# Optimization experiments

Hardware: AMD Instinct MI355X
Metric: run time of the kernel (lower is better)

Reference implementation:

```python
import jax, jax.numpy as jnp
import numpy as np

C = 1024
H = 16
K = 2  # num_states
B, N = 4, 4096


def setup_inputs() -> dict:
    key = jax.random.key(0)
    ks_ = jax.random.split(key, 12)
    s = 1.0 / np.sqrt(C)
    inp = {
        "x": jax.random.normal(ks_[0], (B, N, C), dtype=jnp.float32),
        "Wq": jax.random.normal(ks_[1], (C, C), dtype=jnp.float32) * s,
        "bq": jnp.zeros((C,), dtype=jnp.float32),
        "Wk": jax.random.normal(ks_[2], (K, C, C), dtype=jnp.float32) * s,
        "bk": jnp.zeros((K, C), dtype=jnp.float32),
        "Wv": jax.random.normal(ks_[3], (K, C, C), dtype=jnp.float32) * s,
        "bv": jnp.zeros((K, C), dtype=jnp.float32),
        "Wo": jax.random.normal(ks_[4], (C, C), dtype=jnp.float32) * s,
        "bo": jnp.zeros((C,), dtype=jnp.float32),
        "ln_g": jnp.ones((C,), dtype=jnp.float32),
        "ln_b": jnp.zeros((C,), dtype=jnp.float32),
    }
    return inp


def _heads(t):
    # [..., n, (h d)] -> [..., h, n, d]
    shp = t.shape
    d = shp[-1] // H
    t = t.reshape(shp[:-1] + (H, d))
    return jnp.swapaxes(t, -2, -3)


def reference(x, Wq, bq, Wk, bk, Wv, bv, Wo, bo, ln_g, ln_b):
    dtype = x.dtype
    # residual single-layer projections (ResidualMLP with num_layers=-1)
    q = x + jnp.einsum('bnc,cd->bnd', x, Wq) + bq
    ks = x[None] + jnp.einsum('bnc,kcd->kbnd', x, Wk) + bk[:, None, None, :]
    vs = x[None] + jnp.einsum('bnc,kcd->kbnd', x, Wv) + bv[:, None, None, :]
    q = _heads(q)        # [b,h,n,d]
    ks = _heads(ks)      # [k,b,h,n,d]
    vs = _heads(vs)      # [k,b,h,n,d]
    scale = 1.0 / jnp.sqrt(jnp.asarray(N, dtype=jnp.float32))
    ks = ks.astype(jnp.float32) * scale
    vs = vs.astype(jnp.float32) * scale
    # per-state KV outer-products: [k,b,h,d,e]
    states = jnp.einsum('kbhnd,kbhne->kbhde', ks, vs)
    state = jnp.prod(states, axis=0)  # [b,h,d,e]
    out = jnp.einsum('bhnd,bhde->bhne', q.astype(jnp.float32), state)
    out = out.astype(dtype)
    # [b,h,n,d] -> [b,n,(h d)]
    out = jnp.swapaxes(out, 1, 2).reshape(x.shape[0], x.shape[1], C)
    # LayerNorm
    mu = jnp.mean(out, axis=-1, keepdims=True)
    var = jnp.var(out, axis=-1, keepdims=True)
    out = (out - mu) / jnp.sqrt(var + 1e-5) * ln_g + ln_b
    out = jnp.einsum('bnc,cd->bnd', out, Wo) + bo
    return out
```

## Files before the change

### kernel.cpp

```cpp
#include <hip/hip_runtime.h>
#include <hip/hip_bf16.h>

typedef __attribute__((ext_vector_type(8))) short bf16x8;
typedef __attribute__((ext_vector_type(4))) float f32x4;
typedef __attribute__((ext_vector_type(4))) short s16x4;

__device__ __forceinline__ short f2bf(float f) {
  union { float f; unsigned u; } v; v.f = f;
  unsigned r = v.u + 0x7fffu + ((v.u >> 16) & 1u);
  return (short)(r >> 16);
}

__device__ __forceinline__ float bf2f(short s) {
  union { float f; unsigned u; } v; v.u = ((unsigned)(unsigned short)s) << 16;
  return v.f;
}

#define GLD_LDS(g, l) __builtin_amdgcn_global_load_lds( \
    (const __attribute__((address_space(1))) void*)(g), \
    (__attribute__((address_space(3))) void*)(l), 16, 0, 0)

__global__ __launch_bounds__(256)
void convt_k(const float* __restrict__ x, short* __restrict__ xb,
             short* __restrict__ xbT) {
  __shared__ short tile[64][72];
  const int b = blockIdx.z;
  const int n0 = blockIdx.y * 64;
  const int c0 = blockIdx.x * 64;
  const int t = threadIdx.x;
  const int nl = t >> 4;
  const int c4 = (t & 15) << 2;
  const float* xp = x + ((size_t)b * 4096 + n0) * 1024 + c0;
#pragma unroll
  for (int i = 0; i < 4; ++i) {
    const int n = nl + 16 * i;
    const float4 v = *(const float4*)(xp + (size_t)n * 1024 + c4);
    s16x4 o;
    o[0] = f2bf(v.x); o[1] = f2bf(v.y); o[2] = f2bf(v.z); o[3] = f2bf(v.w);
    *(s16x4*)(&xb[((size_t)b * 4096 + n0 + n) * 1024 + c0 + c4]) = o;
    *(s16x4*)(&tile[n][c4]) = o;
  }
  __syncthreads();
  const int cll = t >> 4;
  const int n4 = (t & 15) << 2;
#pragma unroll
  for (int i = 0; i < 4; ++i) {
    const int c = cll + 16 * i;
    s16x4 o;
    o[0] = tile[n4 + 0][c]; o[1] = tile[n4 + 1][c];
    o[2] = tile[n4 + 2][c]; o[3] = tile[n4 + 3][c];
    *(s16x4*)(&xbT[((size_t)b * 1024 + c0 + c) * 4096 + n0 + n4]) = o;
  }
}

__global__ void twc_k(const float* __restrict__ Wq, const float* __restrict__ Wk,
                      const float* __restrict__ Wv, const float* __restrict__ Wo,
                      const float* __restrict__ lng, short* __restrict__ dst) {
  __shared__ float tile[32][33];
  const int z = blockIdx.z;
  const float* src = (z == 0) ? Wq
                   : (z == 1) ? Wk
                   : (z == 2) ? (Wk + 1048576)
                   : (z == 3) ? Wv
                   : (z == 4) ? (Wv + 1048576)
                   : Wo;
  short* d = dst + (size_t)z * 1048576;
  const int tx = threadIdx.x, ty = threadIdx.y;
  const int c0 = blockIdx.y * 32, d0 = blockIdx.x * 32;
#pragma unroll
  for (int i = 0; i < 4; ++i)
    tile[ty + i * 8][tx] = src[(size_t)(c0 + ty + i * 8) * 1024 + d0 + tx];
  __syncthreads();
#pragma unroll
  for (int i = 0; i < 4; ++i) {
    const int cc = c0 + tx;
    const int dd = d0 + ty + i * 8;
    float v = tile[tx][ty + i * 8];
    if (z < 5) {
      if (cc == dd) v += 1.0f;
    } else {
      v *= lng[cc];
    }
    d[(size_t)dd * 1024 + cc] = f2bf(v);
  }
}

__global__ __launch_bounds__(256)
void colsumT_k(const short* __restrict__ xbT, float* __restrict__ s) {
  const int row = blockIdx.x;
  const int tid = threadIdx.x;
  const short* p = xbT + ((size_t)row << 12);
  float acc = 0.f;
#pragma unroll
  for (int it = 0; it < 2; ++it) {
    const bf16x8 v = *(const bf16x8*)(p + ((tid + it * 256) << 3));
#pragma unroll
    for (int j = 0; j < 8; ++j) acc += bf2f(v[j]);
  }
#pragma unroll
  for (int o = 32; o > 0; o >>= 1) acc += __shfl_down(acc, o);
  __shared__ float red[4];
  if ((tid & 63) == 0) red[tid >> 6] = acc;
  __syncthreads();
  if (tid == 0) s[row] = red[0] + red[1] + red[2] + red[3];
}

__global__ __launch_bounds__(256)
void gemv_k(const short* __restrict__ wt, const float* __restrict__ s,
            float* __restrict__ u, float* __restrict__ w) {
  const int z = blockIdx.z, b = blockIdx.y;
  const int lane = threadIdx.x & 63, wid = threadIdx.x >> 6;
  const short* W = wt + ((size_t)(z + 1) << 20);
  const float* sb = s + b * 1024;
  float* outp = (z < 2) ? (u + (z * 4 + b) * 1024) : (w + ((z - 2) * 4 + b) * 1024);
#pragma unroll 1
  for (int it = 0; it < 16; ++it) {
    const int d = blockIdx.x * 64 + wid * 16 + it;
    const short* row = W + (size_t)d * 1024 + lane * 16;
    float acc = 0.f;
#pragma unroll
    for (int j = 0; j < 16; ++j) acc += bf2f(row[j]) * sb[lane * 16 + j];
#pragma unroll
    for (int o = 32; o > 0; o >>= 1) acc += __shfl_down(acc, o);
    if (lane == 0) outp[d] = acc;
  }
}

__global__ __launch_bounds__(512, 2)
void gramq_k(const short* __restrict__ xb, const short* __restrict__ xbT,
             const short* __restrict__ wtq, const float* __restrict__ bq,
             short* __restrict__ q, float* __restrict__ Pg) {
  extern __shared__ short lds[];
  const int tid = threadIdx.x;
  const int lane = tid & 63;
  const int wv = tid >> 6;
  const int wm = wv >> 2;
  const int wn = wv & 3;
  const int mode = blockIdx.x & 1;
  const int id = blockIdx.x >> 1;
  const int swz = ((id & 7) << 5) + (id >> 3);

  int bm0, bn0, ld, koff;
  const short *Ap, *Bp;
  float* po = nullptr;
  if (mode == 0) {
    const int kz = swz & 3, tl = (swz >> 2) & 15, b = swz >> 6;
    bm0 = (tl >> 2) << 8; bn0 = (tl & 3) << 8;
    ld = 4096; koff = kz << 10;
    Ap = xbT + ((size_t)b << 22);
    Bp = Ap;
    po = Pg + ((size_t)((kz << 2) + b) << 20);
  } else {
    bm0 = (swz & 63) << 8; bn0 = (swz >> 6) << 8;
    ld = 1024; koff = 0;
    Ap = xb; Bp = wtq;
  }

  const int lrow = ((lane >> 3) << 1) | ((lane >> 2) & 1);
  const int kc = ((lane & 3) ^ ((lane >> 3) & 3)) << 3;
  const int cl = lane & 15;
  const int khi = lane >> 4;

  f32x4 acc[8][4];
#pragma unroll
  for (int i = 0; i < 8; ++i)
#pragma unroll
    for (int j = 0; j < 4; ++j) acc[i][j] = f32x4{0.f, 0.f, 0.f, 0.f};

  auto stage = [&](int buf, int t) {
    const int k0 = koff + (t << 5) + kc;
    short* ab = lds + (buf << 14);
    short* bb = ab + 8192;
#pragma unroll
    for (int c = 0; c < 2; ++c) {
      const int un = wv * 2 + c;
      GLD_LDS(Ap + (size_t)(bm0 + (un << 4) + lrow) * ld + k0, ab + (un << 9));
      GLD_LDS(Bp + (size_t)(bn0 + (un << 4) + lrow) * ld + k0, bb + (un << 9));
    }
  };

  auto compute = [&](int buf) {
    const short* ab = lds + (buf << 14);
    const short* bb = ab + 8192;
    bf16x8 af[8], bfr[4];
#pragma unroll
    for (int i = 0; i < 8; ++i) {
      const int R = (wm << 7) + (i << 4) + cl;
      af[i] = *(const bf16x8*)(ab + (R << 5) + ((khi ^ ((R >> 1) & 3)) << 3));
    }
#pragma unroll
    for (int j = 0; j < 4; ++j) {
      const int C = (wn << 6) + (j << 4) + cl;
      bfr[j] = *(const bf16x8*)(bb + (C << 5) + ((khi ^ ((C >> 1) & 3)) << 3));
    }
#pragma unroll
    for (int i = 0; i < 8; ++i)
#pragma unroll
      for (int j = 0; j < 4; ++j)
        acc[i][j] = __builtin_amdgcn_mfma_f32_16x16x32_bf16(af[i], bfr[j], acc[i][j], 0, 0, 0);
  };

  stage(0, 0);
  stage(1, 1);
  asm volatile("s_waitcnt vmcnt(4)" ::: "memory");
  __builtin_amdgcn_s_barrier();
#pragma unroll 1
  for (int t = 0; t < 30; ++t) {
    stage((t + 2) & 3, t + 2);
    compute(t & 3);
    asm volatile("s_waitcnt vmcnt(4)" ::: "memory");
    __builtin_amdgcn_s_barrier();
  }
  compute(2);
  asm volatile("s_waitcnt vmcnt(0)" ::: "memory");
  __builtin_amdgcn_s_barrier();
  compute(3);

  if (mode == 0) {
#pragma unroll
    for (int i = 0; i < 8; ++i)
#pragma unroll
      for (int j = 0; j < 4; ++j) {
        const int col = bn0 + (wn << 6) + (j << 4) + cl;
        const int rowb = bm0 + (wm << 7) + (i << 4) + (khi << 2);
#pragma unroll
        for (int r = 0; r < 4; ++r)
          po[(size_t)(rowb + r) * 1024 + col] = acc[i][j][r];
      }
  } else {
#pragma unroll
    for (int i = 0; i < 8; ++i)
#pragma unroll
      for (int j = 0; j < 4; ++j) {
        const int col = bn0 + (wn << 6) + (j << 4) + cl;
        const int rowb = bm0 + (wm << 7) + (i << 4) + (khi << 2);
        const float bi = bq[col];
#pragma unroll
        for (int r = 0; r < 4; ++r)
          q[(size_t)(rowb + r) * 1024 + col] = f2bf(acc[i][j][r] + bi);
      }
  }
}

__global__ __launch_bounds__(512, 2)
void gemmo_k(const short* __restrict__ A, const short* __restrict__ WT,
             const float* __restrict__ mu, const float* __restrict__ rstd,
             const float* __restrict__ uu, const float* __restrict__ tt,
             float* __restrict__ fout) {
  extern __shared__ short lds[];
  const int tid = threadIdx.x;
  const int lane = tid & 63;
  const int wv = tid >> 6;
  const int wm = wv >> 2;
  const int wn = wv & 3;
  const int swz = ((blockIdx.x & 7) << 5) + (blockIdx.x >> 3);
  const int bm0 = (swz & 63) << 8;
  const int bn0 = (swz >> 6) << 8;

  const int lrow = ((lane >> 3) << 1) | ((lane >> 2) & 1);
  const int kc = ((lane & 3) ^ ((lane >> 3) & 3)) << 3;
  const int cl = lane & 15;
  const int khi = lane >> 4;

  f32x4 acc[8][4];
#pragma unroll
  for (int i = 0; i < 8; ++i)
#pragma unroll
    for (int j = 0; j < 4; ++j) acc[i][j] = f32x4{0.f, 0.f, 0.f, 0.f};

  auto stage = [&](int buf, int t) {
    const int k0 = (t << 5) + kc;
    short* ab = lds + (buf << 14);
    short* bb = ab + 8192;
#pragma unroll
    for (int c = 0; c < 2; ++c) {
      const int un = wv * 2 + c;
      GLD_LDS(A + (size_t)(bm0 + (un << 4) + lrow) * 1024 + k0, ab + (un << 9));
      GLD_LDS(WT + (size_t)(bn0 + (un << 4) + lrow) * 1024 + k0, bb + (un << 9));
    }
  };

  auto compute = [&](int buf) {
    const short* ab = lds + (buf << 14);
    const short* bb = ab + 8192;
    bf16x8 af[8], bfr[4];
#pragma unroll
    for (int i = 0; i < 8; ++i) {
      const int R = (wm << 7) + (i << 4) + cl;
      af[i] = *(const bf16x8*)(ab + (R << 5) + ((khi ^ ((R >> 1) & 3)) << 3));
    }
#pragma unroll
    for (int j = 0; j < 4; ++j) {
      const int C = (wn << 6) + (j << 4) + cl;
      bfr[j] = *(const bf16x8*)(bb + (C << 5) + ((khi ^ ((C >> 1) & 3)) << 3));
    }
#pragma unroll
    for (int i = 0; i < 8; ++i)
#pragma unroll
      for (int j = 0; j < 4; ++j)
        acc[i][j] = __builtin_amdgcn_mfma_f32_16x16x32_bf16(af[i], bfr[j], acc[i][j], 0, 0, 0);
  };

  stage(0, 0);
  stage(1, 1);
  asm volatile("s_waitcnt vmcnt(4)" ::: "memory");
  __builtin_amdgcn_s_barrier();
#pragma unroll 1
  for (int t = 0; t < 30; ++t) {
    stage((t + 2) & 3, t + 2);
    compute(t & 3);
    asm volatile("s_waitcnt vmcnt(4)" ::: "memory");
    __builtin_amdgcn_s_barrier();
  }
  compute(2);
  asm volatile("s_waitcnt vmcnt(0)" ::: "memory");
  __builtin_amdgcn_s_barrier();
  compute(3);

#pragma unroll
  for (int i = 0; i < 8; ++i) {
    const int rowb = bm0 + (wm << 7) + (i << 4) + (khi << 2);
    const float4 m4 = *(const float4*)(mu + rowb);
    const float4 s4 = *(const float4*)(rstd + rowb);
#pragma unroll
    for (int j = 0; j < 4; ++j) {
      const int col = bn0 + (wn << 6) + (j << 4) + cl;
      const float uc = uu[col];
      const float tc = tt[col];
      fout[(size_t)(rowb + 0) * 1024 + col] = s4.x * (acc[i][j][0] - m4.x * uc) + tc;
      fout[(size_t)(rowb + 1) * 1024 + col] = s4.y * (acc[i][j][1] - m4.y * uc) + tc;
      fout[(size_t)(rowb + 2) * 1024 + col] = s4.z * (acc[i][j][2] - m4.z * uc) + tc;
      fout[(size_t)(rowb + 3) * 1024 + col] = s4.w * (acc[i][j][3] - m4.w * uc) + tc;
    }
  }
}

__global__ __launch_bounds__(256)
void greduce_k(const float* __restrict__ Pg, short* __restrict__ G) {
  const int b = blockIdx.x >> 10;
  const int local = ((blockIdx.x & 1023) << 10) + (threadIdx.x << 2);
  float4 a = {0.f, 0.f, 0.f, 0.f};
#pragma unroll
  for (int kz = 0; kz < 4; ++kz) {
    const float4 v = *(const float4*)(Pg + (((size_t)((kz << 2) + b)) << 20) + local);
    a.x += v.x; a.y += v.y; a.z += v.z; a.w += v.w;
  }
  const float sc = 1.0f / 4096.0f;
  s16x4 o;
  o[0] = f2bf(a.x * sc); o[1] = f2bf(a.y * sc);
  o[2] = f2bf(a.z * sc); o[3] = f2bf(a.w * sc);
  *(s16x4*)(G + ((size_t)b << 20) + local) = o;
}

__global__ __launch_bounds__(256)
void gemm128_k(const short* __restrict__ A, const short* __restrict__ Bt,
               short* __restrict__ out) {
  __shared__ short Ab[2][4096];
  __shared__ short Bb[2][4096];
  const int bid = blockIdx.x;
  const int swz = ((bid & 7) << 4) + (bid >> 3);
  const int bm0 = (swz >> 3) << 7;
  const int bn0 = (swz & 7) << 7;
  const short* Bp = Bt + ((size_t)blockIdx.y << 20);
  short* op = out + ((size_t)blockIdx.y << 21);
  const int tid = threadIdx.x, lane = tid & 63, wid = tid >> 6;
  const int wm = (wid >> 1) << 6, wn = (wid & 1) << 6;
  const int lrow = ((lane >> 3) << 1) | ((lane >> 2) & 1);
  const int kc = ((lane & 3) ^ ((lane >> 3) & 3)) << 3;
  const int cl = lane & 15, khi = lane >> 4;

  f32x4 acc[4][4];
#pragma unroll
  for (int i = 0; i < 4; ++i)
#pragma unroll
    for (int j = 0; j < 4; ++j) acc[i][j] = f32x4{0.f, 0.f, 0.f, 0.f};

  auto stage = [&](int buf, int t) {
    const int k0 = (t << 5) + kc;
#pragma unroll
    for (int c = 0; c < 2; ++c) {
      const int un = wid * 2 + c;
      GLD_LDS(A + (size_t)(bm0 + (un << 4) + lrow) * 1024 + k0, &Ab[buf][un << 9]);
      GLD_LDS(Bp + (size_t)(bn0 + (un << 4) + lrow) * 1024 + k0, &Bb[buf][un << 9]);
    }
  };

  stage(0, 0);
  __syncthreads();
#pragma unroll 1
  for (int t = 0; t < 32; ++t) {
    const int cur = t & 1;
    if (t < 31) stage(cur ^ 1, t + 1);
    const short* ab = Ab[cur];
    const short* bb = Bb[cur];
    bf16x8 af[4], bfr[4];
#pragma unroll
    for (int i = 0; i < 4; ++i) {
      const int R = wm + (i << 4) + cl;
      af[i] = *(const bf16x8*)(ab + (R << 5) + ((khi ^ ((R >> 1) & 3)) << 3));
    }
#pragma unroll
    for (int j = 0; j < 4; ++j) {
      const int C = wn + (j << 4) + cl;
      bfr[j] = *(const bf16x8*)(bb + (C << 5) + ((khi ^ ((C >> 1) & 3)) << 3));
    }
#pragma unroll
    for (int i = 0; i < 4; ++i)
#pragma unroll
      for (int j = 0; j < 4; ++j)
        acc[i][j] = __builtin_amdgcn_mfma_f32_16x16x32_bf16(af[i], bfr[j], acc[i][j], 0, 0, 0);
    __syncthreads();
  }

#pragma unroll
  for (int i = 0; i < 4; ++i)
#pragma unroll
    for (int j = 0; j < 4; ++j) {
      const int col = bn0 + wn + (j << 4) + cl;
      const int rowb = bm0 + wm + (i << 4) + (khi << 2);
#pragma unroll
      for (int r = 0; r < 4; ++r)
        op[(size_t)(rowb + r) * 1024 + col] = f2bf(acc[i][j][r]);
    }
}

__global__ __launch_bounds__(256)
void states2_k(const short* __restrict__ wt, const short* __restrict__ Tt,
               float* __restrict__ M) {
  __shared__ short Al[64 * 40];
  __shared__ short Bl[64 * 40];
  const int h = blockIdx.x, b = blockIdx.y, k = blockIdx.z;
  const short* Ap = wt + ((size_t)(1 + k) << 20) + ((size_t)(h * 64) << 10);
  const short* Bp = Tt + ((size_t)b << 21) + ((size_t)(k * 1024 + h * 64) << 10);
  const int tid = threadIdx.x, lane = tid & 63, wid = tid >> 6;
  const int srow = tid >> 2, sch = (tid & 3) << 3;

  f32x4 acc[4];
#pragma unroll
  for (int j = 0; j < 4; ++j) acc[j] = f32x4{0.f, 0.f, 0.f, 0.f};

#pragma unroll 1
  for (int ns = 0; ns < 1024; ns += 32) {
    bf16x8 va = *(const bf16x8*)(Ap + ((size_t)srow << 10) + ns + sch);
    bf16x8 vb = *(const bf16x8*)(Bp + ((size_t)srow << 10) + ns + sch);
    __syncthreads();
    *(bf16x8*)(Al + srow * 40 + sch) = va;
    *(bf16x8*)(Bl + srow * 40 + sch) = vb;
    __syncthreads();
    bf16x8 a = *(const bf16x8*)(Al + (wid * 16 + (lane & 15)) * 40 + ((lane >> 4) << 3));
#pragma unroll
    for (int j = 0; j < 4; ++j) {
      bf16x8 bb = *(const bf16x8*)(Bl + (j * 16 + (lane & 15)) * 40 + ((lane >> 4) << 3));
      acc[j] = __builtin_amdgcn_mfma_f32_16x16x32_bf16(a, bb, acc[j], 0, 0, 0);
    }
  }
  const size_t mb = ((size_t)((k * 4 + b) * 16 + h)) << 12;
  const int r0 = wid * 16 + ((lane >> 4) << 2);
  const int cl = lane & 15;
#pragma unroll
  for (int j = 0; j < 4; ++j)
#pragma unroll
    for (int r = 0; r < 4; ++r)
      M[mb + (size_t)(r0 + r) * 64 + j * 16 + cl] = acc[j][r];
}

__global__ __launch_bounds__(256)
void combine_k(const float* __restrict__ M, const float* __restrict__ u,
               const float* __restrict__ w, const float* __restrict__ bk,
               const float* __restrict__ bv, short* __restrict__ stt) {
  const int bh = blockIdx.x;
  const int b = bh >> 4, h = bh & 15;
  const float invN = 1.0f / 4096.0f;
  for (int t = threadIdx.x; t < 4096; t += 256) {
    const int d = t >> 6, e = t & 63;
    float m[2];
#pragma unroll
    for (int k = 0; k < 2; ++k) {
      const float bkd = bk[k * 1024 + h * 64 + d];
      const float bve = bv[k * 1024 + h * 64 + e];
      const float ud = u[(k * 4 + b) * 1024 + h * 64 + d];
      const float we = w[(k * 4 + b) * 1024 + h * 64 + e];
      m[k] = M[(((size_t)((k * 4 + b) * 16 + h)) << 12) + t]
           + (ud * bve + bkd * we + 4096.f * bkd * bve) * invN;
    }
    stt[(bh << 12) + (e << 6) + d] = f2bf(m[0] * m[1]);
  }
}

__global__ __launch_bounds__(256)
void ut_k(const float* __restrict__ Wo, const float* __restrict__ lng,
          const float* __restrict__ lnb, const float* __restrict__ bo,
          float* __restrict__ u, float* __restrict__ t) {
  const int dl = threadIdx.x & 63;
  const int dd = blockIdx.x * 64 + dl;
  const int part = threadIdx.x >> 6;
  float su = 0.f, st = 0.f;
  for (int c = part * 256; c < part * 256 + 256; ++c) {
    const float w = Wo[(size_t)c * 1024 + dd];
    su += lng[c] * w;
    st += lnb[c] * w;
  }
  __shared__ float rs[4][64], rt[4][64];
  rs[part][dl] = su; rt[part][dl] = st;
  __syncthreads();
  if (part == 0) {
    su = rs[0][dl] + rs[1][dl] + rs[2][dl] + rs[3][dl];
    st = rt[0][dl] + rt[1][dl] + rt[2][dl] + rt[3][dl];
    u[dd] = su;
    t[dd] = st + bo[dd];
  }
}

__global__ __launch_bounds__(256)
void attn_k(const short* __restrict__ q, const short* __restrict__ stt,
            short* __restrict__ oat) {
  __shared__ short Al[128 * 72];
  __shared__ short Bl[64 * 72];
  const int tid = threadIdx.x;
  const int lane = tid & 63;
  const int wid = tid >> 6;
  const int mc = blockIdx.x;
  const int bh = blockIdx.y;
  const int b = bh >> 4, h = bh & 15;
  const size_t qbase = ((size_t)(b * 4096 + mc * 128)) * 1024 + h * 64;
#pragma unroll
  for (int s = 0; s < 4; ++s) {
    const int idx = tid + s * 256;
    const int row = idx >> 3, cc = (idx & 7) << 3;
    *(bf16x8*)(Al + row * 72 + cc) = *(const bf16x8*)(q + qbase + (size_t)row * 1024 + cc);
  }
#pragma unroll
  for (int s = 0; s < 2; ++s) {
    const int idx = tid + s * 256;
    const int row = idx >> 3, cc = (idx & 7) << 3;
    *(bf16x8*)(Bl + row * 72 + cc) = *(const bf16x8*)(stt + (bh << 12) + (row << 6) + cc);
  }
  __syncthreads();
  f32x4 acc[2][4];
#pragma unroll
  for (int i = 0; i < 2; ++i)
#pragma unroll
    for (int j = 0; j < 4; ++j) acc[i][j] = f32x4{0.f, 0.f, 0.f, 0.f};
#pragma unroll
  for (int ks = 0; ks < 2; ++ks) {
    bf16x8 a0 = *(const bf16x8*)(Al + (wid * 32 + (lane & 15)) * 72 + ks * 32 + ((lane >> 4) << 3));
    bf16x8 a1 = *(const bf16x8*)(Al + (wid * 32 + 16 + (lane & 15)) * 72 + ks * 32 + ((lane >> 4) << 3));
#pragma unroll
    for (int j = 0; j < 4; ++j) {
      bf16x8 bb = *(const bf16x8*)(Bl + (j * 16 + (lane & 15)) * 72 + ks * 32 + ((lane >> 4) << 3));
      acc[0][j] = __builtin_amdgcn_mfma_f32_16x16x32_bf16(a0, bb, acc[0][j], 0, 0, 0);
      acc[1][j] = __builtin_amdgcn_mfma_f32_16x16x32_bf16(a1, bb, acc[1][j], 0, 0, 0);
    }
  }
  const int r0 = wid * 32 + ((lane >> 4) << 2);
  const int cl = lane & 15;
#pragma unroll
  for (int i = 0; i < 2; ++i)
#pragma unroll
    for (int j = 0; j < 4; ++j)
#pragma unroll
      for (int r = 0; r < 4; ++r) {
        const int row = b * 4096 + mc * 128 + r0 + i * 16 + r;
        oat[(size_t)row * 1024 + h * 64 + j * 16 + cl] = f2bf(acc[i][j][r]);
      }
}

__global__ __launch_bounds__(256)
void stats_k(const short* __restrict__ oat, float* __restrict__ mu,
             float* __restrict__ rstd) {
  const int row = blockIdx.x;
  const int tid = threadIdx.x;
  const s16x4 v = ((const s16x4*)(oat + (size_t)row * 1024))[tid];
  const float f0 = bf2f(v[0]), f1 = bf2f(v[1]), f2 = bf2f(v[2]), f3 = bf2f(v[3]);
  float s = f0 + f1 + f2 + f3;
  float s2 = f0 * f0 + f1 * f1 + f2 * f2 + f3 * f3;
#pragma unroll
  for (int o = 32; o > 0; o >>= 1) {
    s += __shfl_down(s, o);
    s2 += __shfl_down(s2, o);
  }
  __shared__ float red[8];
  const int wid = tid >> 6, lane = tid & 63;
  if (lane == 0) { red[wid] = s; red[wid + 4] = s2; }
  __syncthreads();
  if (tid == 0) {
    const float ts = red[0] + red[1] + red[2] + red[3];
    const float ts2 = red[4] + red[5] + red[6] + red[7];
    const float m = ts * (1.0f / 1024.0f);
    const float var = ts2 * (1.0f / 1024.0f) - m * m;
    mu[row] = m;
    rstd[row] = rsqrtf(var + 1e-5f);
  }
}

extern "C" void kernel_launch(void* const* d_in, const int* in_sizes, int n_in,
                              void* d_out, int out_size, void* d_ws, size_t ws_size,
                              hipStream_t stream) {
  const float* x = (const float*)d_in[0];
  const float* Wq = (const float*)d_in[1];
  const float* bq = (const float*)d_in[2];
  const float* Wk = (const float*)d_in[3];
  const float* bk = (const float*)d_in[4];
  const float* Wv = (const float*)d_in[5];
  const float* bv = (const float*)d_in[6];
  const float* Wo = (const float*)d_in[7];
  const float* bo = (const float*)d_in[8];
  const float* lng = (const float*)d_in[9];
  const float* lnb = (const float*)d_in[10];

  char* ws = (char*)d_ws;
  short* xb = (short*)(ws + 0);
  short* wt = (short*)(ws + 33554432);
  short* q = (short*)(ws + 46137344);
  short* xbT = (short*)(ws + 79691776);
  short* Gt = (short*)(ws + 113246208);
  short* Tt = (short*)(ws + 121634816);
  float* M = (float*)(ws + 138412032);
  short* stt = (short*)(ws + 142606336);
  float* s = (float*)(ws + 143130624);
  float* u = (float*)(ws + 143147008);
  float* w = (float*)(ws + 143179776);
  float* uu = (float*)(ws + 143212544);
  float* tt = (float*)(ws + 143216640);
  float* mu = (float*)(ws + 143220736);
  float* rstd = (float*)(ws + 143286272);
  float* Pg = (float*)(ws + 143351808);
  short* oat = xb;

  convt_k<<<dim3(16, 64, 4), 256, 0, stream>>>(x, xb, xbT);
  twc_k<<<dim3(32, 32, 6), dim3(32, 8), 0, stream>>>(Wq, Wk, Wv, Wo, lng, wt);
  colsumT_k<<<4096, 256, 0, stream>>>(xbT, s);
  gemv_k<<<dim3(16, 4, 4), 256, 0, stream>>>(wt, s, u, w);

  gramq_k<<<512, 512, 131072, stream>>>(xb, xbT, wt, bq, q, Pg);
  greduce_k<<<4096, 256, 0, stream>>>(Pg, Gt);

  gemm128_k<<<dim3(128, 4), 256, 0, stream>>>(wt + 3145728, Gt, Tt);
  states2_k<<<dim3(16, 4, 2), 256, 0, stream>>>(wt, Tt, M);
  combine_k<<<64, 256, 0, stream>>>(M, u, w, bk, bv, stt);

  ut_k<<<16, 256, 0, stream>>>(Wo, lng, lnb, bo, uu, tt);
  attn_k<<<dim3(32, 64), 256, 0, stream>>>(q, stt, oat);
  stats_k<<<16384, 256, 0, stream>>>(oat, mu, rstd);
  gemmo_k<<<256, 512, 131072, stream>>>(oat, wt + 5242880, mu, rstd, uu, tt,
                                        (float*)d_out);
}
```

Baseline: 266.4 us.

## Fold Q projection into per-batch effective weights and fuse LayerNorm stats

```diff
diff --git a/kernel.cpp b/kernel.cpp
--- a/kernel.cpp
+++ b/kernel.cpp
@@ -55,7 +55,8 @@
 
 __global__ void twc_k(const float* __restrict__ Wq, const float* __restrict__ Wk,
                       const float* __restrict__ Wv, const float* __restrict__ Wo,
-                      const float* __restrict__ lng, short* __restrict__ dst) {
+                      const float* __restrict__ lng, short* __restrict__ dst,
+                      short* __restrict__ wqn) {
   __shared__ float tile[32][33];
   const int z = blockIdx.z;
   const float* src = (z == 0) ? Wq
@@ -68,8 +69,13 @@
   const int tx = threadIdx.x, ty = threadIdx.y;
   const int c0 = blockIdx.y * 32, d0 = blockIdx.x * 32;
 #pragma unroll
-  for (int i = 0; i < 4; ++i)
-    tile[ty + i * 8][tx] = src[(size_t)(c0 + ty + i * 8) * 1024 + d0 + tx];
+  for (int i = 0; i < 4; ++i) {
+    const int cc = c0 + ty + i * 8;
+    const float v = src[(size_t)cc * 1024 + d0 + tx];
+    tile[ty + i * 8][tx] = v;
+    if (z == 0)
+      wqn[(size_t)cc * 1024 + d0 + tx] = f2bf(v + (cc == d0 + tx ? 1.0f : 0.0f));
+  }
   __syncthreads();
 #pragma unroll
   for (int i = 0; i < 4; ++i) {
@@ -126,35 +132,44 @@
   }
 }
 
+__global__ __launch_bounds__(256)
+void ut_k(const float* __restrict__ Wo, const float* __restrict__ lng,
+          const float* __restrict__ lnb, const float* __restrict__ bo,
+          float* __restrict__ u, float* __restrict__ t) {
+  const int dl = threadIdx.x & 63;
+  const int dd = blockIdx.x * 64 + dl;
+  const int part = threadIdx.x >> 6;
+  float su = 0.f, st = 0.f;
+  for (int c = part * 256; c < part * 256 + 256; ++c) {
+    const float w = Wo[(size_t)c * 1024 + dd];
+    su += lng[c] * w;
+    st += lnb[c] * w;
+  }
+  __shared__ float rs[4][64], rt[4][64];
+  rs[part][dl] = su; rt[part][dl] = st;
+  __syncthreads();
+  if (part == 0) {
+    su = rs[0][dl] + rs[1][dl] + rs[2][dl] + rs[3][dl];
+    st = rt[0][dl] + rt[1][dl] + rt[2][dl] + rt[3][dl];
+    u[dd] = su;
+    t[dd] = st + bo[dd];
+  }
+}
+
 __global__ __launch_bounds__(512, 2)
-void gramq_k(const short* __restrict__ xb, const short* __restrict__ xbT,
-             const short* __restrict__ wtq, const float* __restrict__ bq,
-             short* __restrict__ q, float* __restrict__ Pg) {
+void gram_k(const short* __restrict__ xbT, float* __restrict__ Pg) {
   extern __shared__ short lds[];
   const int tid = threadIdx.x;
   const int lane = tid & 63;
   const int wv = tid >> 6;
   const int wm = wv >> 2;
   const int wn = wv & 3;
-  const int mode = blockIdx.x & 1;
-  const int id = blockIdx.x >> 1;
-  const int swz = ((id & 7) << 5) + (id >> 3);
-
-  int bm0, bn0, ld, koff;
-  const short *Ap, *Bp;
-  float* po = nullptr;
-  if (mode == 0) {
-    const int kz = swz & 3, tl = (swz >> 2) & 15, b = swz >> 6;
-    bm0 = (tl >> 2) << 8; bn0 = (tl & 3) << 8;
-    ld = 4096; koff = kz << 10;
-    Ap = xbT + ((size_t)b << 22);
-    Bp = Ap;
-    po = Pg + ((size_t)((kz << 2) + b) << 20);
-  } else {
-    bm0 = (swz & 63) << 8; bn0 = (swz >> 6) << 8;
-    ld = 1024; koff = 0;
-    Ap = xb; Bp = wtq;
-  }
+  const int swz = ((blockIdx.x & 7) << 5) + (blockIdx.x >> 3);
+  const int kz = swz & 3, tl = (swz >> 2) & 15, b = swz >> 6;
+  const int bm0 = (tl >> 2) << 8, bn0 = (tl & 3) << 8;
+  const int koff = kz << 10;
+  const short* Ap = xbT + ((size_t)b << 22);
+  float* po = Pg + ((size_t)((kz << 2) + b) << 20);
 
   const int lrow = ((lane >> 3) << 1) | ((lane >> 2) & 1);
   const int kc = ((lane & 3) ^ ((lane >> 3) & 3)) << 3;
@@ -174,8 +189,8 @@
 #pragma unroll
     for (int c = 0; c < 2; ++c) {
       const int un = wv * 2 + c;
-      GLD_LDS(Ap + (size_t)(bm0 + (un << 4) + lrow) * ld + k0, ab + (un << 9));
-      GLD_LDS(Bp + (size_t)(bn0 + (un << 4) + lrow) * ld + k0, bb + (un << 9));
+      GLD_LDS(Ap + (size_t)(bm0 + (un << 4) + lrow) * 4096 + k0, ab + (un << 9));
+      GLD_LDS(Ap + (size_t)(bn0 + (un << 4) + lrow) * 4096 + k0, bb + (un << 9));
     }
   };
 
@@ -216,37 +231,22 @@
   __builtin_amdgcn_s_barrier();
   compute(3);
 
-  if (mode == 0) {
-#pragma unroll
-    for (int i = 0; i < 8; ++i)
-#pragma unroll
-      for (int j = 0; j < 4; ++j) {
-        const int col = bn0 + (wn << 6) + (j << 4) + cl;
-        const int rowb = bm0 + (wm << 7) + (i << 4) + (khi << 2);
-#pragma unroll
-        for (int r = 0; r < 4; ++r)
-          po[(size_t)(rowb + r) * 1024 + col] = acc[i][j][r];
-      }
-  } else {
-#pragma unroll
-    for (int i = 0; i < 8; ++i)
-#pragma unroll
-      for (int j = 0; j < 4; ++j) {
-        const int col = bn0 + (wn << 6) + (j << 4) + cl;
-        const int rowb = bm0 + (wm << 7) + (i << 4) + (khi << 2);
-        const float bi = bq[col];
-#pragma unroll
-        for (int r = 0; r < 4; ++r)
-          q[(size_t)(rowb + r) * 1024 + col] = f2bf(acc[i][j][r] + bi);
-      }
-  }
+#pragma unroll
+  for (int i = 0; i < 8; ++i)
+#pragma unroll
+    for (int j = 0; j < 4; ++j) {
+      const int col = bn0 + (wn << 6) + (j << 4) + cl;
+      const int rowb = bm0 + (wm << 7) + (i << 4) + (khi << 2);
+#pragma unroll
+      for (int r = 0; r < 4; ++r)
+        po[(size_t)(rowb + r) * 1024 + col] = acc[i][j][r];
+    }
 }
 
 __global__ __launch_bounds__(512, 2)
-void gemmo_k(const short* __restrict__ A, const short* __restrict__ WT,
-             const float* __restrict__ mu, const float* __restrict__ rstd,
-             const float* __restrict__ uu, const float* __restrict__ tt,
-             float* __restrict__ fout) {
+void oat_k(const short* __restrict__ xb, const short* __restrict__ Beff,
+           const float* __restrict__ rq, short* __restrict__ oat,
+           float* __restrict__ musum, float* __restrict__ sqsum) {
   extern __shared__ short lds[];
   const int tid = threadIdx.x;
   const int lane = tid & 63;
@@ -254,8 +254,12 @@
   const int wm = wv >> 2;
   const int wn = wv & 3;
   const int swz = ((blockIdx.x & 7) << 5) + (blockIdx.x >> 3);
-  const int bm0 = (swz & 63) << 8;
-  const int bn0 = (swz >> 6) << 8;
+  const int b = swz >> 6;
+  const int tl = swz & 63;
+  const int bm0 = (tl >> 2) << 8;
+  const int bn0 = (tl & 3) << 8;
+  const short* Ap = xb + ((size_t)b << 22);
+  const short* Bp = Beff + ((size_t)b << 20);
 
   const int lrow = ((lane >> 3) << 1) | ((lane >> 2) & 1);
   const int kc = ((lane & 3) ^ ((lane >> 3) & 3)) << 3;
@@ -275,8 +279,8 @@
 #pragma unroll
     for (int c = 0; c < 2; ++c) {
       const int un = wv * 2 + c;
-      GLD_LDS(A + (size_t)(bm0 + (un << 4) + lrow) * 1024 + k0, ab + (un << 9));
-      GLD_LDS(WT + (size_t)(bn0 + (un << 4) + lrow) * 1024 + k0, bb + (un << 9));
+      GLD_LDS(Ap + (size_t)(bm0 + (un << 4) + lrow) * 1024 + k0, ab + (un << 9));
+      GLD_LDS(Bp + (size_t)(bn0 + (un << 4) + lrow) * 1024 + k0, bb + (un << 9));
     }
   };
 
@@ -320,17 +324,34 @@
 #pragma unroll
   for (int i = 0; i < 8; ++i) {
     const int rowb = bm0 + (wm << 7) + (i << 4) + (khi << 2);
-    const float4 m4 = *(const float4*)(mu + rowb);
-    const float4 s4 = *(const float4*)(rstd + rowb);
+    s16x4 pk[4];
 #pragma unroll
     for (int j = 0; j < 4; ++j) {
       const int col = bn0 + (wn << 6) + (j << 4) + cl;
-      const float uc = uu[col];
-      const float tc = tt[col];
-      fout[(size_t)(rowb + 0) * 1024 + col] = s4.x * (acc[i][j][0] - m4.x * uc) + tc;
-      fout[(size_t)(rowb + 1) * 1024 + col] = s4.y * (acc[i][j][1] - m4.y * uc) + tc;
-      fout[(size_t)(rowb + 2) * 1024 + col] = s4.z * (acc[i][j][2] - m4.z * uc) + tc;
-      fout[(size_t)(rowb + 3) * 1024 + col] = s4.w * (acc[i][j][3] - m4.w * uc) + tc;
+      const float rqc = rq[b * 1024 + col];
+#pragma unroll
+      for (int r = 0; r < 4; ++r) pk[j][r] = f2bf(acc[i][j][r] + rqc);
+#pragma unroll
+      for (int r = 0; r < 4; ++r)
+        oat[(size_t)(b * 4096 + rowb + r) * 1024 + col] = pk[j][r];
+    }
+#pragma unroll
+    for (int r = 0; r < 4; ++r) {
+      float sv = 0.f, sq = 0.f;
+#pragma unroll
+      for (int j = 0; j < 4; ++j) {
+        const float fv = bf2f(pk[j][r]);
+        sv += fv; sq += fv * fv;
+      }
+#pragma unroll
+      for (int m = 1; m < 16; m <<= 1) {
+        sv += __shfl_xor(sv, m);
+        sq += __shfl_xor(sq, m);
+      }
+      if (cl == 0) {
+        atomicAdd(&musum[b * 4096 + rowb + r], sv);
+        atomicAdd(&sqsum[b * 4096 + rowb + r], sq);
+      }
     }
   }
 }
@@ -488,108 +509,150 @@
 }
 
 __global__ __launch_bounds__(256)
-void ut_k(const float* __restrict__ Wo, const float* __restrict__ lng,
-          const float* __restrict__ lnb, const float* __restrict__ bo,
-          float* __restrict__ u, float* __restrict__ t) {
-  const int dl = threadIdx.x & 63;
-  const int dd = blockIdx.x * 64 + dl;
-  const int part = threadIdx.x >> 6;
-  float su = 0.f, st = 0.f;
-  for (int c = part * 256; c < part * 256 + 256; ++c) {
-    const float w = Wo[(size_t)c * 1024 + dd];
-    su += lng[c] * w;
-    st += lnb[c] * w;
-  }
-  __shared__ float rs[4][64], rt[4][64];
-  rs[part][dl] = su; rt[part][dl] = st;
+void weff_k(const short* __restrict__ stt, const short* __restrict__ wqn,
+            const float* __restrict__ bq, short* __restrict__ Beff,
+            float* __restrict__ rq) {
+  __shared__ short S[64][72];
+  const int bh = blockIdx.x;
+  const int b = bh >> 4, h = bh & 15;
+  const int tid = threadIdx.x, lane = tid & 63, wid = tid >> 6;
+  {
+    const int r = tid >> 2, c8 = (tid & 3) << 4;
+    *(bf16x8*)(&S[r][c8]) = *(const bf16x8*)(stt + (bh << 12) + (r << 6) + c8);
+    *(bf16x8*)(&S[r][c8 + 8]) = *(const bf16x8*)(stt + (bh << 12) + (r << 6) + c8 + 8);
+  }
   __syncthreads();
-  if (part == 0) {
-    su = rs[0][dl] + rs[1][dl] + rs[2][dl] + rs[3][dl];
-    st = rt[0][dl] + rt[1][dl] + rt[2][dl] + rt[3][dl];
-    u[dd] = su;
-    t[dd] = st + bo[dd];
-  }
-}
-
-__global__ __launch_bounds__(256)
-void attn_k(const short* __restrict__ q, const short* __restrict__ stt,
-            short* __restrict__ oat) {
-  __shared__ short Al[128 * 72];
-  __shared__ short Bl[64 * 72];
+  if (wid == 0) {
+    float acc = 0.f;
+#pragma unroll 1
+    for (int d = 0; d < 64; ++d) acc += bq[h * 64 + d] * bf2f(S[lane][d]);
+    rq[b * 1024 + h * 64 + lane] = acc;
+  }
+  const int cl = lane & 15, khi = lane >> 4;
+  bf16x8 af[4][2];
+#pragma unroll
+  for (int mi = 0; mi < 4; ++mi)
+#pragma unroll
+    for (int kk = 0; kk < 2; ++kk)
+      af[mi][kk] = *(const bf16x8*)(&S[mi * 16 + cl][kk * 32 + khi * 8]);
+  const short* wq = wqn + h * 64;
+  short* bdst = Beff + ((size_t)b << 20) + ((size_t)(h * 64) << 10);
+#pragma unroll 1
+  for (int nf = 0; nf < 16; ++nf) {
+    const int c0 = wid * 256 + nf * 16;
+    const bf16x8 bf0 = *(const bf16x8*)(wq + (size_t)(c0 + cl) * 1024 + khi * 8);
+    const bf16x8 bf1 = *(const bf16x8*)(wq + (size_t)(c0 + cl) * 1024 + 32 + khi * 8);
+    f32x4 a4[4];
+#pragma unroll
+    for (int mi = 0; mi < 4; ++mi) {
+      a4[mi] = f32x4{0.f, 0.f, 0.f, 0.f};
+      a4[mi] = __builtin_amdgcn_mfma_f32_16x16x32_bf16(af[mi][0], bf0, a4[mi], 0, 0, 0);
+      a4[mi] = __builtin_amdgcn_mfma_f32_16x16x32_bf16(af[mi][1], bf1, a4[mi], 0, 0, 0);
+    }
+#pragma unroll
+    for (int mi = 0; mi < 4; ++mi)
+#pragma unroll
+      for (int r = 0; r < 4; ++r)
+        bdst[(size_t)(mi * 16 + khi * 4 + r) * 1024 + c0 + cl] = f2bf(a4[mi][r]);
+  }
+}
+
+__global__ __launch_bounds__(512, 2)
+void gemmo_k(const short* __restrict__ A, const short* __restrict__ WT,
+             const float* __restrict__ musum, const float* __restrict__ sqsum,
+             const float* __restrict__ uu, const float* __restrict__ tt,
+             float* __restrict__ fout) {
+  extern __shared__ short lds[];
   const int tid = threadIdx.x;
   const int lane = tid & 63;
-  const int wid = tid >> 6;
-  const int mc = blockIdx.x;
-  const int bh = blockIdx.y;
-  const int b = bh >> 4, h = bh & 15;
-  const size_t qbase = ((size_t)(b * 4096 + mc * 128)) * 1024 + h * 64;
-#pragma unroll
-  for (int s = 0; s < 4; ++s) {
-    const int idx = tid + s * 256;
-    const int row = idx >> 3, cc = (idx & 7) << 3;
-    *(bf16x8*)(Al + row * 72 + cc) = *(const bf16x8*)(q + qbase + (size_t)row * 1024 + cc);
-  }
-#pragma unroll
-  for (int s = 0; s < 2; ++s) {
-    const int idx = tid + s * 256;
-    const int row = idx >> 3, cc = (idx & 7) << 3;
-    *(bf16x8*)(Bl + row * 72 + cc) = *(const bf16x8*)(stt + (bh << 12) + (row << 6) + cc);
-  }
-  __syncthreads();
-  f32x4 acc[2][4];
-#pragma unroll
-  for (int i = 0; i < 2; ++i)
+  const int wv = tid >> 6;
+  const int wm = wv >> 2;
+  const int wn = wv & 3;
+  const int swz = ((blockIdx.x & 7) << 5) + (blockIdx.x >> 3);
+  const int bm0 = (swz & 63) << 8;
+  const int bn0 = (swz >> 6) << 8;
+
+  const int lrow = ((lane >> 3) << 1) | ((lane >> 2) & 1);
+  const int kc = ((lane & 3) ^ ((lane >> 3) & 3)) << 3;
+  const int cl = lane & 15;
+  const int khi = lane >> 4;
+
+  f32x4 acc[8][4];
+#pragma unroll
+  for (int i = 0; i < 8; ++i)
 #pragma unroll
     for (int j = 0; j < 4; ++j) acc[i][j] = f32x4{0.f, 0.f, 0.f, 0.f};
-#pragma unroll
-  for (int ks = 0; ks < 2; ++ks) {
-    bf16x8 a0 = *(const bf16x8*)(Al + (wid * 32 + (lane & 15)) * 72 + ks * 32 + ((lane >> 4) << 3));
-    bf16x8 a1 = *(const bf16x8*)(Al + (wid * 32 + 16 + (lane & 15)) * 72 + ks * 32 + ((lane >> 4) << 3));
-#pragma unroll
-    for (int j = 0; j < 4; ++j) {
-      bf16x8 bb = *(const bf16x8*)(Bl + (j * 16 + (lane & 15)) * 72 + ks * 32 + ((lane >> 4) << 3));
-      acc[0][j] = __builtin_amdgcn_mfma_f32_16x16x32_bf16(a0, bb, acc[0][j], 0, 0, 0);
-      acc[1][j] = __builtin_amdgcn_mfma_f32_16x16x32_bf16(a1, bb, acc[1][j], 0, 0, 0);
-    }
-  }
-  const int r0 = wid * 32 + ((lane >> 4) << 2);
-  const int cl = lane & 15;
-#pragma unroll
-  for (int i = 0; i < 2; ++i)
-#pragma unroll
-    for (int j = 0; j < 4; ++j)
-#pragma unroll
-      for (int r = 0; r < 4; ++r) {
-        const int row = b * 4096 + mc * 128 + r0 + i * 16 + r;
-        oat[(size_t)row * 1024 + h * 64 + j * 16 + cl] = f2bf(acc[i][j][r]);
-      }
-}
-
-__global__ __launch_bounds__(256)
-void stats_k(const short* __restrict__ oat, float* __restrict__ mu,
-             float* __restrict__ rstd) {
-  const int row = blockIdx.x;
-  const int tid = threadIdx.x;
-  const s16x4 v = ((const s16x4*)(oat + (size_t)row * 1024))[tid];
-  const float f0 = bf2f(v[0]), f1 = bf2f(v[1]), f2 = bf2f(v[2]), f3 = bf2f(v[3]);
-  float s = f0 + f1 + f2 + f3;
-  float s2 = f0 * f0 + f1 * f1 + f2 * f2 + f3 * f3;
-#pragma unroll
-  for (int o = 32; o > 0; o >>= 1) {
-    s += __shfl_down(s, o);
-    s2 += __shfl_down(s2, o);
-  }
-  __shared__ float red[8];
-  const int wid = tid >> 6, lane = tid & 63;
-  if (lane == 0) { red[wid] = s; red[wid + 4] = s2; }
-  __syncthreads();
-  if (tid == 0) {
-    const float ts = red[0] + red[1] + red[2] + red[3];
-    const float ts2 = red[4] + red[5] + red[6] + red[7];
-    const float m = ts * (1.0f / 1024.0f);
-    const float var = ts2 * (1.0f / 1024.0f) - m * m;
-    mu[row] = m;
-    rstd[row] = rsqrtf(var + 1e-5f);
+
+  auto stage = [&](int buf, int t) {
+    const int k0 = (t << 5) + kc;
+    short* ab = lds + (buf << 14);
+    short* bb = ab + 8192;
+#pragma unroll
+    for (int c = 0; c < 2; ++c) {
+      const int un = wv * 2 + c;
+      GLD_LDS(A + (size_t)(bm0 + (un << 4) + lrow) * 1024 + k0, ab + (un << 9));
+      GLD_LDS(WT + (size_t)(bn0 + (un << 4) + lrow) * 1024 + k0, bb + (un << 9));
+    }
+  };
+
+  auto compute = [&](int buf) {
+    const short* ab = lds + (buf << 14);
+    const short* bb = ab + 8192;
+    bf16x8 af[8], bfr[4];
+#pragma unroll
+    for (int i = 0; i < 8; ++i) {
+      const int R = (wm << 7) + (i << 4) + cl;
+      af[i] = *(const bf16x8*)(ab + (R << 5) + ((khi ^ ((R >> 1) & 3)) << 3));
+    }
+#pragma unroll
+    for (int j = 0; j < 4; ++j) {
+      const int C = (wn << 6) + (j << 4) + cl;
+      bfr[j] = *(const bf16x8*)(bb + (C << 5) + ((khi ^ ((C >> 1) & 3)) << 3));
+    }
+#pragma unroll
+    for (int i = 0; i < 8; ++i)
+#pragma unroll
+      for (int j = 0; j < 4; ++j)
+        acc[i][j] = __builtin_amdgcn_mfma_f32_16x16x32_bf16(af[i], bfr[j], acc[i][j], 0, 0, 0);
+  };
+
+  stage(0, 0);
+  stage(1, 1);
+  asm volatile("s_waitcnt vmcnt(4)" ::: "memory");
+  __builtin_amdgcn_s_barrier();
+#pragma unroll 1
+  for (int t = 0; t < 30; ++t) {
+    stage((t + 2) & 3, t + 2);
+    compute(t & 3);
+    asm volatile("s_waitcnt vmcnt(4)" ::: "memory");
+    __builtin_amdgcn_s_barrier();
+  }
+  compute(2);
+  asm volatile("s_waitcnt vmcnt(0)" ::: "memory");
+  __builtin_amdgcn_s_barrier();
+  compute(3);
+
+#pragma unroll
+  for (int i = 0; i < 8; ++i) {
+    const int rowb = bm0 + (wm << 7) + (i << 4) + (khi << 2);
+    const float4 ms = *(const float4*)(musum + rowb);
+    const float4 qs = *(const float4*)(sqsum + rowb);
+    float mu[4], rs[4];
+    mu[0] = ms.x * (1.0f / 1024.0f); mu[1] = ms.y * (1.0f / 1024.0f);
+    mu[2] = ms.z * (1.0f / 1024.0f); mu[3] = ms.w * (1.0f / 1024.0f);
+    rs[0] = rsqrtf(fmaxf(qs.x * (1.0f / 1024.0f) - mu[0] * mu[0], 0.f) + 1e-5f);
+    rs[1] = rsqrtf(fmaxf(qs.y * (1.0f / 1024.0f) - mu[1] * mu[1], 0.f) + 1e-5f);
+    rs[2] = rsqrtf(fmaxf(qs.z * (1.0f / 1024.0f) - mu[2] * mu[2], 0.f) + 1e-5f);
+    rs[3] = rsqrtf(fmaxf(qs.w * (1.0f / 1024.0f) - mu[3] * mu[3], 0.f) + 1e-5f);
+#pragma unroll
+    for (int j = 0; j < 4; ++j) {
+      const int col = bn0 + (wn << 6) + (j << 4) + cl;
+      const float uc = uu[col];
+      const float tc = tt[col];
+#pragma unroll
+      for (int r = 0; r < 4; ++r)
+        fout[(size_t)(rowb + r) * 1024 + col] = rs[r] * (acc[i][j][r] - mu[r] * uc) + tc;
+    }
   }
 }
 
@@ -611,37 +674,39 @@
   char* ws = (char*)d_ws;
   short* xb = (short*)(ws + 0);
   short* wt = (short*)(ws + 33554432);
-  short* q = (short*)(ws + 46137344);
+  short* wqn = (short*)(ws + 46137344);
+  short* Beff = (short*)(ws + 48234496);
+  float* rq = (float*)(ws + 56623104);
+  float* musum = (float*)(ws + 56639488);
+  float* sqsum = (float*)(ws + 56705024);
+  float* s = (float*)(ws + 56770560);
+  float* u = (float*)(ws + 56786944);
+  float* w = (float*)(ws + 56819712);
+  float* uu = (float*)(ws + 56852480);
+  float* tt = (float*)(ws + 56856576);
   short* xbT = (short*)(ws + 79691776);
   short* Gt = (short*)(ws + 113246208);
   short* Tt = (short*)(ws + 121634816);
   float* M = (float*)(ws + 138412032);
   short* stt = (short*)(ws + 142606336);
-  float* s = (float*)(ws + 143130624);
-  float* u = (float*)(ws + 143147008);
-  float* w = (float*)(ws + 143179776);
-  float* uu = (float*)(ws + 143212544);
-  float* tt = (float*)(ws + 143216640);
-  float* mu = (float*)(ws + 143220736);
-  float* rstd = (float*)(ws + 143286272);
   float* Pg = (float*)(ws + 143351808);
-  short* oat = xb;
-
+  short* oat = xbT;
+
+  hipMemsetAsync(musum, 0, 131072, stream);
   convt_k<<<dim3(16, 64, 4), 256, 0, stream>>>(x, xb, xbT);
-  twc_k<<<dim3(32, 32, 6), dim3(32, 8), 0, stream>>>(Wq, Wk, Wv, Wo, lng, wt);
+  twc_k<<<dim3(32, 32, 6), dim3(32, 8), 0, stream>>>(Wq, Wk, Wv, Wo, lng, wt, wqn);
   colsumT_k<<<4096, 256, 0, stream>>>(xbT, s);
   gemv_k<<<dim3(16, 4, 4), 256, 0, stream>>>(wt, s, u, w);
-
-  gramq_k<<<512, 512, 131072, stream>>>(xb, xbT, wt, bq, q, Pg);
+  ut_k<<<16, 256, 0, stream>>>(Wo, lng, lnb, bo, uu, tt);
+
+  gram_k<<<256, 512, 131072, stream>>>(xbT, Pg);
   greduce_k<<<4096, 256, 0, stream>>>(Pg, Gt);
-
   gemm128_k<<<dim3(128, 4), 256, 0, stream>>>(wt + 3145728, Gt, Tt);
   states2_k<<<dim3(16, 4, 2), 256, 0, stream>>>(wt, Tt, M);
   combine_k<<<64, 256, 0, stream>>>(M, u, w, bk, bv, stt);
-
-  ut_k<<<16, 256, 0, stream>>>(Wo, lng, lnb, bo, uu, tt);
-  attn_k<<<dim3(32, 64), 256, 0, stream>>>(q, stt, oat);
-  stats_k<<<16384, 256, 0, stream>>>(oat, mu, rstd);
-  gemmo_k<<<256, 512, 131072, stream>>>(oat, wt + 5242880, mu, rstd, uu, tt,
+  weff_k<<<64, 256, 0, stream>>>(stt, wqn, bq, Beff, rq);
+
+  oat_k<<<256, 512, 131072, stream>>>(xb, Beff, rq, oat, musum, sqsum);
+  gemmo_k<<<256, 512, 131072, stream>>>(oat, wt + 5242880, musum, sqsum, uu, tt,
                                         (float*)d_out);
 }
```

Result: slower. 283.8 us (+6.5%).
